# Optimization experiments

Hardware: AMD Instinct MI355X
Metric: run time of the kernel (lower is better)

The kernel has to match this reference:

```python
import jax, jax.numpy as jnp
import numpy as np

N = 100000   # nodes
E = 1600000  # edges
D = 128      # feature dim
DO = 3       # out_head target dim
C = 50000    # centers


def setup_inputs() -> dict:
    key = jax.random.key(0)
    k1, k2, k3, k4 = jax.random.split(key, 4)
    H = jax.random.normal(k1, (N, D), dtype=jnp.float32)
    W = jax.random.normal(k2, (D, DO), dtype=jnp.float32) / np.sqrt(D)
    b = jnp.zeros((DO,), dtype=jnp.float32)
    target = jax.random.normal(k3, (N, DO), dtype=jnp.float32)
    edge_index = jax.random.randint(k4, (2, E), 0, N, dtype=jnp.int32)
    centers = jnp.arange(C, dtype=jnp.int32)  # distinct center node ids
    return {"H": H, "W": W, "b": b, "target": target,
            "edge_index": edge_index, "centers": centers}


def reference(H, W, b, target, edge_index, centers):
    # Vectorized equivalent of the per-center Python loop:
    # for each edge (s, d): if s is a center, pair (owner(s), d) contributes
    # mean-squared error of out_head(H[d]) vs target[d]; then per-center mean,
    # then mean over all centers (empty centers contribute 0 via cnt clamp).
    n_nodes = H.shape[0]
    n_centers = centers.shape[0]
    # node id -> center slot (n_centers == "not a center" sentinel)
    owner_of = jnp.full((n_nodes,), n_centers, dtype=jnp.int32)
    owner_of = owner_of.at[centers].set(jnp.arange(n_centers, dtype=jnp.int32))
    src, dst = edge_index[0], edge_index[1]
    owners = owner_of[src]              # [E]
    mask = owners < n_centers           # [E] edge rooted at a center

    z_frontier = H[dst]                 # [E, D] neighbor-feature gather
    y_hat = z_frontier @ W + b          # [E, DO] out_head (linear)
    y_true = target[dst]                # [E, DO]
    err = jnp.mean((y_hat - y_true) ** 2, axis=-1)  # [E]
    errm = jnp.where(mask, err, jnp.zeros((), err.dtype))

    # segment-mean per center; sentinel bucket n_centers dropped
    loss_sum = jax.ops.segment_sum(errm, owners, num_segments=n_centers + 1)[:n_centers]
    cnt = jax.ops.segment_sum(mask.astype(err.dtype), owners,
                              num_segments=n_centers + 1)[:n_centers]
    aux_loss = jnp.mean(loss_sum / jnp.maximum(cnt, 1.0))
    return aux_loss
```

## Files before the change

kernel.cpp:

```cpp
#include <hip/hip_runtime.h>


#define CNT_SHIFT 44
#define ERR_SCALE 67108864.0f
#define BKT_SHIFT 8
#define BKT_SIZE  256
#define P2B       256
#define BKT_THR   1024
#define STASH     6272
#define PREF_STRIDE 200

__device__ __forceinline__ int owner_fn(int s, bool fast, int C,
                                        const int* __restrict__ arr_idx,
                                        const int* __restrict__ centers) {
    if (fast) return (s < C) ? s : -1;
    int i = arr_idx[s];
    return ((unsigned)i < (unsigned)C && centers[i] == s) ? i : -1;
}

__global__ __launch_bounds__(256)
void prep_err_kernel(const float* __restrict__ H, const float* __restrict__ W,
                     const float* __restrict__ b, const float* __restrict__ target,
                     const int* __restrict__ centers,
                     float* __restrict__ err_node,
                     int* __restrict__ arr_idx,
                     int* __restrict__ flagpart,
                     float* __restrict__ out,
                     int N, int C, int NBV, int out_size) {
    __shared__ int ok;
    const int t = threadIdx.x;
    const int gtid = blockIdx.x * 256 + t;

    if (blockIdx.x < NBV) {
        if (t == 0) ok = 1;
        __syncthreads();
        bool mism = false;
        if (gtid < C) {
            int c = centers[gtid];
            arr_idx[c] = gtid;
            mism = (c != gtid);
        }
        if (__ballot(mism) != 0ull && (t & 63) == 0) atomicAnd(&ok, 0);
        __syncthreads();
        if (t == 0) flagpart[blockIdx.x] = ok;
    }
    if (gtid < out_size) out[gtid] = 0.f;

    const int node = gtid;
    if (node >= N) return;
    const float4* Hr = reinterpret_cast<const float4*>(H) + (size_t)node * 32;

    float a0 = 0.f, a1 = 0.f, a2 = 0.f;
    float4 ra[8], rb[8];

    #define LOADG(arr, g)                                                   \
        { _Pragma("unroll")                                                 \
          for (int i = 0; i < 8; ++i) arr[i] = Hr[(g) * 8 + i]; }
    #define COMPG(arr, g)                                                   \
        { _Pragma("unroll")                                                 \
          for (int i = 0; i < 8; ++i) {                                     \
              float hx[4] = {arr[i].x, arr[i].y, arr[i].z, arr[i].w};       \
              _Pragma("unroll")                                             \
              for (int e = 0; e < 4; ++e) {                                 \
                  const int k = (g) * 32 + i * 4 + e;                       \
                  a0 += hx[e] * W[k * 3 + 0];                               \
                  a1 += hx[e] * W[k * 3 + 1];                               \
                  a2 += hx[e] * W[k * 3 + 2];                               \
              }                                                             \
          } }

    LOADG(ra, 0) LOADG(rb, 1)
    COMPG(ra, 0) LOADG(ra, 2)
    COMPG(rb, 1) LOADG(rb, 3)
    COMPG(ra, 2) COMPG(rb, 3)
    #undef LOADG
    #undef COMPG

    float e0 = a0 + b[0] - target[(size_t)node * 3 + 0];
    float e1 = a1 + b[1] - target[(size_t)node * 3 + 1];
    float e2 = a2 + b[2] - target[(size_t)node * 3 + 2];
    err_node[node] = (e0 * e0 + e1 * e1 + e2 * e2) * (1.0f / 3.0f);
}

__global__ __launch_bounds__(BKT_THR)
void bucketize_kernel(const int* __restrict__ eidx,
                      const int* __restrict__ centers,
                      const int* __restrict__ arr_idx,
                      const int* __restrict__ flagpart,
                      unsigned short* __restrict__ pref_g,
                      unsigned int* __restrict__ pairs,
                      int E, int C, int NB, int NBV) {
    __shared__ unsigned int stash[STASH];
    __shared__ int          src_c[STASH];
    __shared__ unsigned int hist[256];
    __shared__ unsigned int scan[256];
    __shared__ unsigned int total_sh;
    __shared__ int okf;
    const int t = threadIdx.x;

    if (t == 0) okf = 1;
    if (t < 256) hist[t] = 0u;
    __syncthreads();
    bool my_ok = (t < NBV) ? (flagpart[t] != 0) : true;
    if (__ballot(!my_ok) != 0ull && (t & 63) == 0) atomicAnd(&okf, 0);
    __syncthreads();
    const bool fast = (okf != 0);

    const int E4     = E >> 2;
    const int chunk4 = (E4 + P2B - 1) / P2B;
    const int c0     = blockIdx.x * chunk4;
    const int c1     = min(E4, c0 + chunk4);
    const int4* r0 = reinterpret_cast<const int4*>(eidx);
    const int4* r1 = reinterpret_cast<const int4*>(eidx + E);

    for (int i = c0 + t; i < c1; i += BKT_THR) {
        int4 s4 = r0[i];
        reinterpret_cast<int4*>(src_c)[i - c0] = s4;
        int ss[4] = {s4.x, s4.y, s4.z, s4.w};
        #pragma unroll
        for (int k = 0; k < 4; ++k) {
            int o = owner_fn(ss[k], fast, C, arr_idx, centers);
            if (o >= 0) atomicAdd(&hist[(unsigned)o >> BKT_SHIFT], 1u);
        }
    }
    __syncthreads();
    if (t < 256) scan[t] = hist[t];
    __syncthreads();
    for (int off = 1; off < 256; off <<= 1) {
        unsigned v = (t < 256 && t >= off) ? scan[t - off] : 0u;
        __syncthreads();
        if (t < 256 && t >= off) scan[t] += v;
        __syncthreads();
    }
    if (t < 256) {
        unsigned pre = (t == 0) ? 0u : scan[t - 1];
        hist[t] = pre;
        if (t <= NB)
            pref_g[(size_t)blockIdx.x * PREF_STRIDE + t] = (unsigned short)pre;
    }
    if (t == 0) total_sh = scan[255];
    __syncthreads();
    for (int i = c0 + t; i < c1; i += BKT_THR) {
        int4 d4 = r1[i];
        int4 s4 = reinterpret_cast<const int4*>(src_c)[i - c0];
        int ss[4] = {s4.x, s4.y, s4.z, s4.w};
        int dd[4] = {d4.x, d4.y, d4.z, d4.w};
        #pragma unroll
        for (int k = 0; k < 4; ++k) {
            int o = owner_fn(ss[k], fast, C, arr_idx, centers);
            if (o >= 0) {
                unsigned bk = (unsigned)o >> BKT_SHIFT;
                unsigned pos = atomicAdd(&hist[bk], 1u);
                stash[pos] = (((unsigned)o & (BKT_SIZE - 1)) << 17)
                           | (unsigned)dd[k];
            }
        }
    }
    __syncthreads();
    {
        unsigned nvec = (total_sh + 3u) >> 2;
        uint4*       dg = reinterpret_cast<uint4*>(pairs + (size_t)blockIdx.x * STASH);
        const uint4* sg = reinterpret_cast<const uint4*>(stash);
        for (unsigned i = t; i < nvec; i += BKT_THR) dg[i] = sg[i];
    }
}

__global__ __launch_bounds__(1024)
void reduce_kernel(const unsigned int* __restrict__ pairs,
                   const unsigned short* __restrict__ pref_g,
                   const float* __restrict__ err_node,
                   float* __restrict__ out, int C, float invC) {
    __shared__ unsigned long long bins[BKT_SIZE];
    __shared__ float wsum[16];
    const int bk = blockIdx.x, t = threadIdx.x;
    if (t < BKT_SIZE) bins[t] = 0ull;
    __syncthreads();
    {
        const int seg = t >> 2;
        const int j   = t & 3;
        const size_t pb = (size_t)seg * PREF_STRIDE;
        unsigned start = pref_g[pb + bk];
        unsigned end   = pref_g[pb + bk + 1];
        const unsigned int* reg = pairs + (size_t)seg * STASH;
        for (unsigned i = start + j; i < end; i += 4) {
            unsigned p = reg[i];
            float err = err_node[p & 0x1FFFFu];
            atomicAdd(&bins[p >> 17],
                      (1ull << CNT_SHIFT) + (unsigned long long)(err * ERR_SCALE));
        }
    }
    __syncthreads();
    float term = 0.f;
    if (t < BKT_SIZE) {
        int center = bk * BKT_SIZE + t;
        if (center < C) {
            unsigned long long u = bins[t];
            float cnt = (float)(u >> CNT_SHIFT);
            float es  = (float)(u & ((1ull << CNT_SHIFT) - 1)) * (1.0f / ERR_SCALE);
            term = es / fmaxf(cnt, 1.0f);
        }
    }
    #pragma unroll
    for (int m = 32; m > 0; m >>= 1) term += __shfl_down(term, m, 64);
    if ((t & 63) == 0) wsum[t >> 6] = term;
    __syncthreads();
    if (t == 0) {
        float s = 0.f;
        #pragma unroll
        for (int w = 0; w < 16; ++w) s += wsum[w];
        atomicAdd(out, s * invC);
    }
}

__global__ __launch_bounds__(256)
void fb_err_kernel(const float* __restrict__ H, const float* __restrict__ W,
                   const float* __restrict__ b, const float* __restrict__ target,
                   const int* __restrict__ centers,
                   float* __restrict__ err_node, int* __restrict__ arr_idx,
                   float* __restrict__ out, int N, int C, int D, int DO,
                   int out_size) {
    int gtid = blockIdx.x * blockDim.x + threadIdx.x;
    if (gtid < C) arr_idx[centers[gtid]] = gtid;
    if (gtid < out_size) out[gtid] = 0.f;
    if (gtid < N) {
        float acc = 0.f;
        for (int j = 0; j < DO; ++j) {
            float a = b[j];
            for (int r = 0; r < D; ++r)
                a += H[(size_t)gtid * D + r] * W[(size_t)r * DO + j];
            float e = a - target[(size_t)gtid * DO + j];
            acc += e * e;
        }
        err_node[gtid] = acc / (float)DO;
    }
}

__global__ void fb_edge_kernel(const int* __restrict__ eidx,
                               const int* __restrict__ arr_idx,
                               const int* __restrict__ centers,
                               const float* __restrict__ err_node,
                               unsigned long long* __restrict__ binsg,
                               int E, int C) {
    int e = blockIdx.x * blockDim.x + threadIdx.x;
    if (e >= E) return;
    int s = eidx[e];
    int o = owner_fn(s, false, C, arr_idx, centers);
    if (o >= 0) {
        int d = eidx[E + e];
        unsigned long long add = (1ull << CNT_SHIFT)
                               + (unsigned long long)(err_node[d] * ERR_SCALE);
        atomicAdd(&binsg[o], add);
    }
}

__global__ void fb_finalize_kernel(const unsigned long long* __restrict__ binsg,
                                   float* __restrict__ out, int C) {
    int i = blockIdx.x * blockDim.x + threadIdx.x;
    float term = 0.f;
    if (i < C) {
        unsigned long long u = binsg[i];
        float cnt = (float)(u >> CNT_SHIFT);
        float es  = (float)(u & ((1ull << CNT_SHIFT) - 1)) * (1.0f / ERR_SCALE);
        term = es / fmaxf(cnt, 1.0f);
    }
    #pragma unroll
    for (int m = 32; m > 0; m >>= 1) term += __shfl_down(term, m, 64);
    __shared__ float wsum[4];
    if ((threadIdx.x & 63) == 0) wsum[threadIdx.x >> 6] = term;
    __syncthreads();
    if (threadIdx.x == 0)
        atomicAdd(out, (wsum[0] + wsum[1] + wsum[2] + wsum[3]) / (float)C);
}

extern "C" void kernel_launch(void* const* d_in, const int* in_sizes, int n_in,
                              void* d_out, int out_size, void* d_ws, size_t ws_size,
                              hipStream_t stream) {
    const float* H      = (const float*)d_in[0];
    const float* W      = (const float*)d_in[1];
    const float* b      = (const float*)d_in[2];
    const float* target = (const float*)d_in[3];
    const int*   eidx   = (const int*)d_in[4];
    const int*   ctrs   = (const int*)d_in[5];

    const int DO = in_sizes[2];
    const int D  = in_sizes[1] / DO;
    const int N  = in_sizes[0] / D;
    const int E  = in_sizes[4] / 2;
    const int C  = in_sizes[5];
    const int NB  = (C + BKT_SIZE - 1) >> BKT_SHIFT;
    const int NBV = (C + 255) / 256;
    const int EB  = (N + 255) / 256;

    size_t off = 0;
    auto take = [&](size_t bytes) {
        void* p = (char*)d_ws + off;
        off = (off + bytes + 255) & ~255ull;
        return p;
    };
    float*          err_node = (float*)take((size_t)N * 4);
    int*            arr_idx  = (int*)take((size_t)N * 4);
    int*            flagpart = (int*)take((size_t)NBV * 4);
    unsigned short* pref_g   = (unsigned short*)take((size_t)P2B * PREF_STRIDE * 2);
    unsigned int*   pairs    = (unsigned int*)((char*)d_ws + off);
    size_t need = off + (size_t)P2B * STASH * 4;

    int chunk_edges = 4 * ((E / 4 + P2B - 1) / P2B);
    bool fits = (ws_size >= need) && (NB + 1 <= PREF_STRIDE) && (NBV <= BKT_THR) &&
                (NBV <= EB) && (N < (1 << 17)) && ((E & 3) == 0) &&
                (chunk_edges <= STASH) && (D == 128) && (DO == 3) && (out_size >= 1);
    if (fits) {
        prep_err_kernel<<<EB, 256, 0, stream>>>(H, W, b, target, ctrs,
                                                err_node, arr_idx, flagpart,
                                                (float*)d_out, N, C, NBV,
                                                out_size);
        bucketize_kernel<<<P2B, BKT_THR, 0, stream>>>(eidx, ctrs, arr_idx,
                                                      flagpart, pref_g, pairs,
                                                      E, C, NB, NBV);
        reduce_kernel<<<NB, 1024, 0, stream>>>(pairs, pref_g, err_node,
                                               (float*)d_out, C, 1.0f / (float)C);
    } else {
        unsigned long long* binsg = (unsigned long long*)((char*)d_ws + off);
        hipMemsetAsync(binsg, 0, (size_t)C * 8, stream);
        int thr = 256;
        fb_err_kernel<<<(max(N, C) + thr - 1) / thr, thr, 0, stream>>>(
            H, W, b, target, ctrs, err_node, arr_idx, (float*)d_out,
            N, C, D, DO, out_size);
        fb_edge_kernel<<<(E + thr - 1) / thr, thr, 0, stream>>>(
            eidx, arr_idx, ctrs, err_node, binsg, E, C);
        fb_finalize_kernel<<<(C + thr - 1) / thr, thr, 0, stream>>>(
            binsg, (float*)d_out, C);
    }
}
```

Before: 34.24 us.

## Use per-wave bucket histograms and wave-shuffle scan in bucketize kernel

```diff
diff --git a/kernel.cpp b/kernel.cpp
--- a/kernel.cpp
+++ b/kernel.cpp
@@ -7,6 +7,7 @@
 #define BKT_SIZE  256
 #define P2B       256
 #define BKT_THR   1024
+#define NWAVE     16
 #define STASH     6272
 #define PREF_STRIDE 200
 
@@ -91,15 +92,17 @@
                       unsigned int* __restrict__ pairs,
                       int E, int C, int NB, int NBV) {
     __shared__ unsigned int stash[STASH];
-    __shared__ int          src_c[STASH];
-    __shared__ unsigned int hist[256];
-    __shared__ unsigned int scan[256];
+    __shared__ unsigned int hw[NWAVE * 256];
+    __shared__ unsigned int binv[256];
     __shared__ unsigned int total_sh;
     __shared__ int okf;
     const int t = threadIdx.x;
+    const int w = t >> 6;
 
     if (t == 0) okf = 1;
-    if (t < 256) hist[t] = 0u;
+    #pragma unroll
+    for (int i = 0; i < (NWAVE * 256) / BKT_THR; ++i)
+        hw[t + i * BKT_THR] = 0u;
     __syncthreads();
     bool my_ok = (t < NBV) ? (flagpart[t] != 0) : true;
     if (__ballot(!my_ok) != 0ull && (t & 63) == 0) atomicAnd(&okf, 0);
@@ -112,37 +115,60 @@
     const int c1     = min(E4, c0 + chunk4);
     const int4* r0 = reinterpret_cast<const int4*>(eidx);
     const int4* r1 = reinterpret_cast<const int4*>(eidx + E);
+    unsigned int* myh = hw + w * 256;
 
     for (int i = c0 + t; i < c1; i += BKT_THR) {
         int4 s4 = r0[i];
-        reinterpret_cast<int4*>(src_c)[i - c0] = s4;
         int ss[4] = {s4.x, s4.y, s4.z, s4.w};
         #pragma unroll
         for (int k = 0; k < 4; ++k) {
             int o = owner_fn(ss[k], fast, C, arr_idx, centers);
-            if (o >= 0) atomicAdd(&hist[(unsigned)o >> BKT_SHIFT], 1u);
-        }
-    }
-    __syncthreads();
-    if (t < 256) scan[t] = hist[t];
-    __syncthreads();
-    for (int off = 1; off < 256; off <<= 1) {
-        unsigned v = (t < 256 && t >= off) ? scan[t - off] : 0u;
-        __syncthreads();
-        if (t < 256 && t >= off) scan[t] += v;
-        __syncthreads();
-    }
+            if (o >= 0) atomicAdd(&myh[(unsigned)o >> BKT_SHIFT], 1u);
+        }
+    }
+    __syncthreads();
     if (t < 256) {
-        unsigned pre = (t == 0) ? 0u : scan[t - 1];
-        hist[t] = pre;
+        unsigned run = 0;
+        #pragma unroll
+        for (int ww = 0; ww < NWAVE; ++ww) {
+            unsigned v = hw[ww * 256 + t];
+            hw[ww * 256 + t] = run;
+            run += v;
+        }
+        binv[t] = run;
+    }
+    __syncthreads();
+    if (t < 64) {
+        unsigned v0 = binv[4 * t], v1 = binv[4 * t + 1];
+        unsigned v2 = binv[4 * t + 2], v3 = binv[4 * t + 3];
+        unsigned s0 = v0, s01 = v0 + v1, s012 = s01 + v2;
+        unsigned lt = s012 + v3;
+        unsigned sum = lt;
+        #pragma unroll
+        for (int d = 1; d < 64; d <<= 1) {
+            unsigned x = __shfl_up(sum, d, 64);
+            if (t >= d) sum += x;
+        }
+        unsigned excl = sum - lt;
+        binv[4 * t]     = excl;
+        binv[4 * t + 1] = excl + s0;
+        binv[4 * t + 2] = excl + s01;
+        binv[4 * t + 3] = excl + s012;
+        if (t == 63) total_sh = sum;
+    }
+    __syncthreads();
+    if (t < 256) {
+        unsigned bb = binv[t];
         if (t <= NB)
-            pref_g[(size_t)blockIdx.x * PREF_STRIDE + t] = (unsigned short)pre;
-    }
-    if (t == 0) total_sh = scan[255];
+            pref_g[(size_t)blockIdx.x * PREF_STRIDE + t] = (unsigned short)bb;
+        #pragma unroll
+        for (int ww = 0; ww < NWAVE; ++ww)
+            hw[ww * 256 + t] += bb;
+    }
     __syncthreads();
     for (int i = c0 + t; i < c1; i += BKT_THR) {
+        int4 s4 = r0[i];
         int4 d4 = r1[i];
-        int4 s4 = reinterpret_cast<const int4*>(src_c)[i - c0];
         int ss[4] = {s4.x, s4.y, s4.z, s4.w};
         int dd[4] = {d4.x, d4.y, d4.z, d4.w};
         #pragma unroll
@@ -150,7 +176,7 @@
             int o = owner_fn(ss[k], fast, C, arr_idx, centers);
             if (o >= 0) {
                 unsigned bk = (unsigned)o >> BKT_SHIFT;
-                unsigned pos = atomicAdd(&hist[bk], 1u);
+                unsigned pos = atomicAdd(&myh[bk], 1u);
                 stash[pos] = (((unsigned)o & (BKT_SIZE - 1)) << 17)
                            | (unsigned)dd[k];
             }
```

Result: no change. 34.13 us (-0.3%).
